# Kernel tuning notes

Measured on AMD Instinct MI355X. Metric: run time of the kernel, lower is better.

The kernel has to match this reference:

```python
import jax, jax.numpy as jnp
import numpy as np

DATA_SHAPE = (4, 32, 32)
K_EMBED_DIM = 64


def _local_stats(zf):
    # zf: [B, N]; torch std/var use ddof=1; torch.median returns lower median (sorted index (N-1)//2)
    n = zf.shape[1]
    mean = jnp.mean(zf, axis=1)
    var = jnp.var(zf, axis=1, ddof=1)
    std = jnp.sqrt(var)
    mn = jnp.min(zf, axis=1)
    mx = jnp.max(zf, axis=1)
    med = jnp.sort(zf, axis=1)[:, (n - 1) // 2]
    l2 = jnp.sqrt(jnp.sum(zf * zf, axis=1))
    l1 = jnp.sum(jnp.abs(zf), axis=1)
    pos = jnp.sum(zf > 0, axis=1).astype(zf.dtype)
    neg = jnp.sum(zf < 0, axis=1).astype(zf.dtype)
    return jnp.stack([mean, std, mn, mx, med, var, l2, l1, pos, neg], axis=1)


def _sinusoidal_embedding(k, dim):
    half = dim // 2
    freqs = jnp.exp(jnp.arange(half, dtype=jnp.float32) * (-np.log(10000.0) / (half - 1)))
    e = k * freqs
    return jnp.concatenate([jnp.sin(e), jnp.cos(e)], axis=0)  # [dim]


def _pos_encoding(t, f, s, max_scales):
    t = jnp.float32(t); f = jnp.float32(f)
    return jnp.stack([jnp.sin(0.1 * t), jnp.cos(0.1 * t), jnp.sin(0.1 * f), jnp.cos(0.1 * f),
                      jnp.float32(s) / jnp.float32(max_scales)])


def setup_inputs() -> dict:
    key = jax.random.key(0)
    ks = jax.random.split(key, 8)
    B = 8192
    input_dim = int(np.prod(DATA_SHAPE)) + K_EMBED_DIM + 5 + 10  # 4175
    def xavier(k, fan_in, fan_out):
        bound = np.sqrt(6.0 / (fan_in + fan_out))
        return jax.random.uniform(k, (fan_in, fan_out), jnp.float32, -bound, bound)
    return {
        "z_local": jax.random.normal(ks[0], (B,) + DATA_SHAPE, jnp.float32),
        "k": 500, "t": 10, "f": 20, "s": 2, "max_scales": 4,
        "W1": xavier(ks[1], input_dim, 256), "b1": jnp.zeros((256,), jnp.float32),
        "W2": xavier(ks[2], 256, 128), "b2": jnp.zeros((128,), jnp.float32),
        "W3": xavier(ks[3], 128, 64), "b3": jnp.zeros((64,), jnp.float32),
        "W4": xavier(ks[4], 64, 5), "b4": jnp.zeros((5,), jnp.float32),
    }


def reference(z_local, k, t, f, s, max_scales, W1, b1, W2, b2, W3, b3, W4, b4):
    B = z_local.shape[0]
    zf = z_local.reshape(B, -1)  # [B, 4096] == prod(data_shape), no pad/trim needed
    k_embed = _sinusoidal_embedding(k, K_EMBED_DIM)           # [64]
    pos_enc = _pos_encoding(t, f, s, max_scales)              # [5]
    stats = _local_stats(zf)                                  # [B, 10]
    feats = jnp.concatenate([
        zf,
        jnp.broadcast_to(k_embed[None, :], (B, K_EMBED_DIM)),
        jnp.broadcast_to(pos_enc[None, :], (B, 5)),
        stats,
    ], axis=1)
    h = jax.nn.relu(feats @ W1 + b1)
    h = jax.nn.relu(h @ W2 + b2)
    h = jax.nn.relu(h @ W3 + b3)
    logits = h @ W4 + b4
    return jax.nn.softmax(logits, axis=-1)
```

## Files before the change

kernel.cpp:

```cpp
#include <hip/hip_runtime.h>
#include <math.h>
#include <stdint.h>

#define DFEAT 4096
#define AS1 __attribute__((address_space(1)))
#define AS3 __attribute__((address_space(3)))

typedef _Float16 f16x8 __attribute__((ext_vector_type(8)));
typedef float f32x4 __attribute__((ext_vector_type(4)));

__global__ __launch_bounds__(256, 4) void stats_kernel(const float* __restrict__ z,
                                                       float* __restrict__ stats)
{
    const int lane = threadIdx.x & 63;
    const int wv   = threadIdx.x >> 6;
    const int row  = blockIdx.x * 4 + wv;
    const float* zr = z + (size_t)row * DFEAT;

    unsigned keys[64];
    float sum = 0.f, ss = 0.f, l1 = 0.f;
    float mn = INFINITY, mx = -INFINITY;
    int pos = 0, neg = 0;

    #pragma unroll
    for (int j = 0; j < 16; ++j) {
        float4 v = reinterpret_cast<const float4*>(zr)[lane + j * 64];
        float vv[4] = {v.x, v.y, v.z, v.w};
        #pragma unroll
        for (int e = 0; e < 4; ++e) {
            float x = vv[e];
            sum += x; ss += x * x; l1 += fabsf(x);
            mn = fminf(mn, x); mx = fmaxf(mx, x);
            pos += (x > 0.f) ? 1 : 0;
            neg += (x < 0.f) ? 1 : 0;
            unsigned u = __float_as_uint(x);
            keys[j * 4 + e] = (u & 0x80000000u) ? ~u : (u | 0x80000000u);
        }
    }

    #pragma unroll
    for (int off = 1; off < 64; off <<= 1) {
        sum += __shfl_xor(sum, off);
        ss  += __shfl_xor(ss,  off);
        l1  += __shfl_xor(l1,  off);
        mn = fminf(mn, __shfl_xor(mn, off));
        mx = fmaxf(mx, __shfl_xor(mx, off));
        pos += __shfl_xor(pos, off);
        neg += __shfl_xor(neg, off);
    }

    unsigned lo = 0u;
    const int t = (DFEAT - 1) / 2;
    #pragma unroll 1
    for (int b = 31; b >= 0; --b) {
        const unsigned mid = lo | (1u << b);
        int cnt = 0;
        #pragma unroll
        for (int i = 0; i < 64; ++i) cnt += (keys[i] < mid) ? 1 : 0;
        #pragma unroll
        for (int off = 1; off < 64; off <<= 1) cnt += __shfl_xor(cnt, off);
        if (cnt <= t) lo = mid;
    }

    if (lane == 0) {
        const float med = (lo & 0x80000000u) ? __uint_as_float(lo ^ 0x80000000u)
                                             : __uint_as_float(~lo);
        const float n = (float)DFEAT;
        const float mean = sum / n;
        const float var = (ss - sum * sum / n) / (n - 1.f);
        float* sp = stats + (size_t)row * 10;
        sp[0] = mean;
        sp[1] = sqrtf(var);
        sp[2] = mn;
        sp[3] = mx;
        sp[4] = med;
        sp[5] = var;
        sp[6] = sqrtf(ss);
        sp[7] = l1;
        sp[8] = (float)pos;
        sp[9] = (float)neg;
    }
}

__global__ __launch_bounds__(256) void split_kernel(const float* __restrict__ W1,
                                                    char* __restrict__ img)
{
    const int c   = blockIdx.x;
    const int col = threadIdx.x;
    const int k0  = c * 32;
    _Float16 h16[32], l16[32];
    #pragma unroll
    for (int kk = 0; kk < 32; ++kk) {
        float w = W1[(size_t)(k0 + kk) * 256 + col];
        _Float16 h = (_Float16)w;
        float rr = (w - (float)h) * 2048.f;
        h16[kk] = h;
        l16[kk] = (_Float16)rr;
    }
    char* base = img + (size_t)c * 32768;
    const int sw = (col >> 1) & 3;
    #pragma unroll
    for (int g = 0; g < 4; ++g) {
        f16x8 vh, vl;
        #pragma unroll
        for (int j = 0; j < 8; ++j) { vh[j] = h16[g * 8 + j]; vl[j] = l16[g * 8 + j]; }
        const int off = col * 64 + ((g ^ sw) << 4);
        *reinterpret_cast<f16x8*>(base + off)         = vh;
        *reinterpret_cast<f16x8*>(base + 16384 + off) = vl;
    }
}

__global__ __launch_bounds__(256) void prep_kernel(const int* kp, const int* tp,
                                                   const int* fp, const int* sp,
                                                   const int* msp,
                                                   const float* __restrict__ W1,
                                                   const float* __restrict__ b1,
                                                   float* __restrict__ cbias)
{
    __shared__ float ke[64];
    __shared__ float pe[5];
    const int tid = threadIdx.x;
    if (tid < 32) {
        const float c = (float)(-log(10000.0) / 31.0);
        const float freq = expf((float)tid * c);
        const float e = (float)(*kp) * freq;
        const double ed = (double)e;
        ke[tid]      = (float)sin(ed);
        ke[tid + 32] = (float)cos(ed);
    }
    if (tid == 0) {
        const float tf = (float)(*tp), ff = (float)(*fp);
        pe[0] = (float)sin((double)(0.1f * tf));
        pe[1] = (float)cos((double)(0.1f * tf));
        pe[2] = (float)sin((double)(0.1f * ff));
        pe[3] = (float)cos((double)(0.1f * ff));
        pe[4] = (float)(*sp) / (float)(*msp);
    }
    __syncthreads();
    float acc = b1[tid];
    #pragma unroll 8
    for (int i = 0; i < 64; ++i) acc += ke[i] * W1[(size_t)(4096 + i) * 256 + tid];
    #pragma unroll
    for (int i = 0; i < 5; ++i)  acc += pe[i] * W1[(size_t)(4160 + i) * 256 + tid];
    cbias[tid] = acc;
}

__global__ __launch_bounds__(256, 1) void mlp_kernel(
    const float* __restrict__ z, const char* __restrict__ img,
    const float* __restrict__ W1, const float* __restrict__ W2,
    const float* __restrict__ b2, const float* __restrict__ W3,
    const float* __restrict__ b3, const float* __restrict__ W4,
    const float* __restrict__ b4, const float* __restrict__ stats,
    const float* __restrict__ cbias, float* __restrict__ out)
{
    __shared__ char lds[65536];

    const int tid  = threadIdx.x;
    const int wv   = tid >> 6;
    const int r    = wv >> 1;
    const int cg   = wv & 1;
    const int lane = tid & 63;
    const int q    = lane & 15;
    const int g    = lane >> 4;
    const int row0 = blockIdx.x * 32;

    f32x4 acc0[8], acc1[8];
    #pragma unroll
    for (int f = 0; f < 8; ++f) {
        acc0[f] = (f32x4){0.f, 0.f, 0.f, 0.f};
        acc1[f] = (f32x4){0.f, 0.f, 0.f, 0.f};
    }

    const float* arow = z + (size_t)(row0 + 16 * r + q) * DFEAT + g * 8;
    const int sw = (q >> 1) & 3;

#define STAGE_B(T, DST) do {                                                   \
        const char* gsrc_ = img + (size_t)(T) * 32768 + wv * 8192 + lane * 16; \
        char* ldst_ = (DST) + wv * 8192;                                       \
        _Pragma("unroll")                                                      \
        for (int i_ = 0; i_ < 8; ++i_) {                                       \
            __builtin_amdgcn_global_load_lds(                                  \
                (const AS1 void*)(gsrc_ + i_ * 1024),                          \
                (AS3 void*)(ldst_ + i_ * 1024), 16, 0, 0);                     \
        }                                                                      \
    } while (0)

    float af[8];
    {
        STAGE_B(0, lds);
        float4 v0 = *reinterpret_cast<const float4*>(arow);
        float4 v1 = *reinterpret_cast<const float4*>(arow + 4);
        af[0] = v0.x; af[1] = v0.y; af[2] = v0.z; af[3] = v0.w;
        af[4] = v1.x; af[5] = v1.y; af[6] = v1.z; af[7] = v1.w;
    }
    __syncthreads();

    for (int tt = 0; tt < 128; ++tt) {
        char* buf  = lds + ((tt & 1) << 15);
        char* nbuf = lds + (((tt + 1) & 1) << 15);

        if (tt + 1 < 128) STAGE_B(tt + 1, nbuf);

        f16x8 ah, al;
        #pragma unroll
        for (int j = 0; j < 8; ++j) {
            _Float16 h = (_Float16)af[j];
            ah[j] = h;
            al[j] = (_Float16)((af[j] - (float)h) * 2048.f);
        }

        if (tt + 1 < 128) {
            const float* an = arow + (tt + 1) * 32;
            float4 v0 = *reinterpret_cast<const float4*>(an);
            float4 v1 = *reinterpret_cast<const float4*>(an + 4);
            af[0] = v0.x; af[1] = v0.y; af[2] = v0.z; af[3] = v0.w;
            af[4] = v1.x; af[5] = v1.y; af[6] = v1.z; af[7] = v1.w;
        }

        #pragma unroll
        for (int f = 0; f < 8; ++f) {
            const int colf = 128 * cg + 16 * f + q;
            const int off  = colf * 64 + ((g ^ sw) << 4);
            f16x8 bh = *reinterpret_cast<const f16x8*>(buf + off);
            f16x8 bl = *reinterpret_cast<const f16x8*>(buf + 16384 + off);
            acc0[f] = __builtin_amdgcn_mfma_f32_16x16x32_f16(ah, bh, acc0[f], 0, 0, 0);
            acc1[f] = __builtin_amdgcn_mfma_f32_16x16x32_f16(ah, bl, acc1[f], 0, 0, 0);
            acc1[f] = __builtin_amdgcn_mfma_f32_16x16x32_f16(al, bh, acc1[f], 0, 0, 0);
        }
        __syncthreads();
    }

    float* W1s_s   = reinterpret_cast<float*>(lds + 40000);
    float* stats_s = reinterpret_cast<float*>(lds + 50240);
    float* cb_s    = reinterpret_cast<float*>(lds + 51520);
    float* Hs      = reinterpret_cast<float*>(lds);

    for (int i = tid; i < 2560; i += 256) {
        const int s = i >> 8, cc = i & 255;
        W1s_s[i] = W1[(size_t)(4165 + s) * 256 + cc];
    }
    for (int i = tid; i < 320; i += 256)
        stats_s[i] = stats[(size_t)row0 * 10 + i];
    cb_s[tid] = cbias[tid];
    __syncthreads();

    #pragma unroll
    for (int j = 0; j < 4; ++j) {
        const int m = g * 4 + j;
        const int grow = 16 * r + m;
        float s10[10];
        #pragma unroll
        for (int s = 0; s < 10; ++s) s10[s] = stats_s[grow * 10 + s];
        #pragma unroll
        for (int f = 0; f < 8; ++f) {
            const int colf = 128 * cg + 16 * f + q;
            float h = acc0[f][j] + acc1[f][j] * (1.f / 2048.f) + cb_s[colf];
            #pragma unroll
            for (int s = 0; s < 10; ++s) h += s10[s] * W1s_s[s * 256 + colf];
            Hs[grow * 257 + colf] = fmaxf(h, 0.f);
        }
    }
    __syncthreads();

    float* H2 = reinterpret_cast<float*>(lds + 40000);
    {
        const int rr = tid >> 3;
        const int c0 = (tid & 7) * 16;
        float a2[16];
        #pragma unroll
        for (int i = 0; i < 16; ++i) a2[i] = b2[c0 + i];
        for (int k = 0; k < 256; ++k) {
            const float hv = Hs[rr * 257 + k];
            const float4 w0 = *reinterpret_cast<const float4*>(W2 + (size_t)k * 128 + c0);
            const float4 w1 = *reinterpret_cast<const float4*>(W2 + (size_t)k * 128 + c0 + 4);
            const float4 w2 = *reinterpret_cast<const float4*>(W2 + (size_t)k * 128 + c0 + 8);
            const float4 w3 = *reinterpret_cast<const float4*>(W2 + (size_t)k * 128 + c0 + 12);
            const float wvv[16] = {w0.x,w0.y,w0.z,w0.w, w1.x,w1.y,w1.z,w1.w,
                                   w2.x,w2.y,w2.z,w2.w, w3.x,w3.y,w3.z,w3.w};
            #pragma unroll
            for (int i = 0; i < 16; ++i) a2[i] += hv * wvv[i];
        }
        __syncthreads();
        #pragma unroll
        for (int i = 0; i < 16; ++i)
            H2[rr * 129 + c0 + i] = fmaxf(a2[i], 0.f);
    }
    __syncthreads();

    float* H3 = reinterpret_cast<float*>(lds + 56512);
    {
        const int rr = tid >> 3;
        const int c0 = (tid & 7) * 8;
        float a3[8];
        #pragma unroll
        for (int i = 0; i < 8; ++i) a3[i] = b3[c0 + i];
        for (int k = 0; k < 128; ++k) {
            const float hv = H2[rr * 129 + k];
            const float4 w0 = *reinterpret_cast<const float4*>(W3 + (size_t)k * 64 + c0);
            const float4 w1 = *reinterpret_cast<const float4*>(W3 + (size_t)k * 64 + c0 + 4);
            const float wvv[8] = {w0.x,w0.y,w0.z,w0.w, w1.x,w1.y,w1.z,w1.w};
            #pragma unroll
            for (int i = 0; i < 8; ++i) a3[i] += hv * wvv[i];
        }
        #pragma unroll
        for (int i = 0; i < 8; ++i)
            H3[rr * 65 + c0 + i] = fmaxf(a3[i], 0.f);
    }
    __syncthreads();

    if (tid < 32) {
        const int rr = tid;
        float lg[5];
        #pragma unroll
        for (int j = 0; j < 5; ++j) lg[j] = b4[j];
        for (int k = 0; k < 64; ++k) {
            const float hv = H3[rr * 65 + k];
            #pragma unroll
            for (int j = 0; j < 5; ++j) lg[j] += hv * W4[k * 5 + j];
        }
        float m = lg[0];
        #pragma unroll
        for (int j = 1; j < 5; ++j) m = fmaxf(m, lg[j]);
        float e[5], s = 0.f;
        #pragma unroll
        for (int j = 0; j < 5; ++j) { e[j] = expf(lg[j] - m); s += e[j]; }
        float* op = out + (size_t)(row0 + rr) * 5;
        #pragma unroll
        for (int j = 0; j < 5; ++j) op[j] = e[j] / s;
    }
#undef STAGE_B
}

extern "C" void kernel_launch(void* const* d_in, const int* in_sizes, int n_in,
                              void* d_out, int out_size, void* d_ws, size_t ws_size,
                              hipStream_t stream)
{
    const float* z   = (const float*)d_in[0];
    const int*   kp  = (const int*)d_in[1];
    const int*   tp  = (const int*)d_in[2];
    const int*   fp  = (const int*)d_in[3];
    const int*   sp  = (const int*)d_in[4];
    const int*   msp = (const int*)d_in[5];
    const float* W1  = (const float*)d_in[6];
    const float* b1  = (const float*)d_in[7];
    const float* W2  = (const float*)d_in[8];
    const float* b2  = (const float*)d_in[9];
    const float* W3  = (const float*)d_in[10];
    const float* b3  = (const float*)d_in[11];
    const float* W4  = (const float*)d_in[12];
    const float* b4  = (const float*)d_in[13];
    float* out = (float*)d_out;

    const int B = in_sizes[0] / DFEAT;
    float* ws_stats = (float*)d_ws;
    float* ws_cbias = ws_stats + (size_t)B * 10;
    char*  ws_img   = (char*)(ws_cbias + 256);

    hipLaunchKernelGGL(stats_kernel, dim3(B / 4), dim3(256), 0, stream, z, ws_stats);
    hipLaunchKernelGGL(split_kernel, dim3(128), dim3(256), 0, stream, W1, ws_img);
    hipLaunchKernelGGL(prep_kernel, dim3(1), dim3(256), 0, stream,
                       kp, tp, fp, sp, msp, W1, b1, ws_cbias);
    hipLaunchKernelGGL(mlp_kernel, dim3(B / 32), dim3(256), 0, stream,
                       z, ws_img, W1, W2, b2, W3, b3, W4, b4,
                       ws_stats, ws_cbias, out);
}
```

Before: 519.4 us.

## Deepen MLP B-operand pipeline to four LDS stages and split stats per block

The main GEMM loop moves from a double-buffered LDS ring with a full __syncthreads per chunk to a four-slot ring that keeps three chunks of W1 in flight, using explicit vmcnt waits and raw barriers, with A-row loads prefetched two chunks ahead. The aim is to hide global-to-LDS latency better in the memory-bound first layer, at the cost of 128 KB of LDS per block. Separately, the stats kernel now gives each row a whole 256-thread block instead of one wavefront. This cuts per-thread register keys from 64 to 16 but adds two block barriers per radix-select bit.

After: 504.5 us. 1.03x faster.

```diff
diff --git a/kernel.cpp b/kernel.cpp
--- a/kernel.cpp
+++ b/kernel.cpp
@@ -9,22 +9,26 @@
 typedef _Float16 f16x8 __attribute__((ext_vector_type(8)));
 typedef float f32x4 __attribute__((ext_vector_type(4)));
 
-__global__ __launch_bounds__(256, 4) void stats_kernel(const float* __restrict__ z,
-                                                       float* __restrict__ stats)
-{
-    const int lane = threadIdx.x & 63;
-    const int wv   = threadIdx.x >> 6;
-    const int row  = blockIdx.x * 4 + wv;
+__global__ __launch_bounds__(256) void stats_kernel(const float* __restrict__ z,
+                                                    float* __restrict__ stats)
+{
+    const int row  = blockIdx.x;
+    const int tid  = threadIdx.x;
+    const int lane = tid & 63;
+    const int wv   = tid >> 6;
+    __shared__ float wred[4][7];
+    __shared__ int   wcnt[4];
+
     const float* zr = z + (size_t)row * DFEAT;
 
-    unsigned keys[64];
+    unsigned keys[16];
     float sum = 0.f, ss = 0.f, l1 = 0.f;
     float mn = INFINITY, mx = -INFINITY;
     int pos = 0, neg = 0;
 
     #pragma unroll
-    for (int j = 0; j < 16; ++j) {
-        float4 v = reinterpret_cast<const float4*>(zr)[lane + j * 64];
+    for (int j = 0; j < 4; ++j) {
+        float4 v = reinterpret_cast<const float4*>(zr)[tid + j * 256];
         float vv[4] = {v.x, v.y, v.z, v.w};
         #pragma unroll
         for (int e = 0; e < 4; ++e) {
@@ -48,37 +52,54 @@
         pos += __shfl_xor(pos, off);
         neg += __shfl_xor(neg, off);
     }
+    if (lane == 0) {
+        wred[wv][0] = sum; wred[wv][1] = ss; wred[wv][2] = l1;
+        wred[wv][3] = mn;  wred[wv][4] = mx;
+        wred[wv][5] = (float)pos; wred[wv][6] = (float)neg;
+    }
+    __syncthreads();
 
     unsigned lo = 0u;
-    const int t = (DFEAT - 1) / 2;
     #pragma unroll 1
     for (int b = 31; b >= 0; --b) {
         const unsigned mid = lo | (1u << b);
-        int cnt = 0;
-        #pragma unroll
-        for (int i = 0; i < 64; ++i) cnt += (keys[i] < mid) ? 1 : 0;
-        #pragma unroll
-        for (int off = 1; off < 64; off <<= 1) cnt += __shfl_xor(cnt, off);
-        if (cnt <= t) lo = mid;
-    }
-
-    if (lane == 0) {
+        int c = 0;
+        #pragma unroll
+        for (int i = 0; i < 16; ++i) c += (keys[i] < mid) ? 1 : 0;
+        #pragma unroll
+        for (int off = 1; off < 64; off <<= 1) c += __shfl_xor(c, off);
+        if (lane == 0) wcnt[wv] = c;
+        __syncthreads();
+        const int tot = wcnt[0] + wcnt[1] + wcnt[2] + wcnt[3];
+        if (tot <= 2047) lo = mid;
+        __syncthreads();
+    }
+
+    if (tid == 0) {
+        float fsum = 0.f, fss = 0.f, fl1 = 0.f, fpos = 0.f, fneg = 0.f;
+        float fmn = INFINITY, fmx = -INFINITY;
+        #pragma unroll
+        for (int w = 0; w < 4; ++w) {
+            fsum += wred[w][0]; fss += wred[w][1]; fl1 += wred[w][2];
+            fmn = fminf(fmn, wred[w][3]); fmx = fmaxf(fmx, wred[w][4]);
+            fpos += wred[w][5]; fneg += wred[w][6];
+        }
         const float med = (lo & 0x80000000u) ? __uint_as_float(lo ^ 0x80000000u)
                                              : __uint_as_float(~lo);
         const float n = (float)DFEAT;
-        const float mean = sum / n;
-        const float var = (ss - sum * sum / n) / (n - 1.f);
+        const float mean = fsum / n;
+        const float var = (fss - fsum * fsum / n) / (n - 1.f);
         float* sp = stats + (size_t)row * 10;
         sp[0] = mean;
         sp[1] = sqrtf(var);
-        sp[2] = mn;
-        sp[3] = mx;
+        sp[2] = fmn;
+        sp[3] = fmx;
         sp[4] = med;
         sp[5] = var;
-        sp[6] = sqrtf(ss);
-        sp[7] = l1;
-        sp[8] = (float)pos;
-        sp[9] = (float)neg;
+        sp[6] = sqrtf(fss);
+        sp[7] = fl1;
+        sp[8] = fpos;
+        sp[9] = fneg;
     }
 }
 
@@ -153,7 +174,7 @@
     const float* __restrict__ b4, const float* __restrict__ stats,
     const float* __restrict__ cbias, float* __restrict__ out)
 {
-    __shared__ char lds[65536];
+    __shared__ char lds[131072];
 
     const int tid  = threadIdx.x;
     const int wv   = tid >> 6;
@@ -174,61 +195,65 @@
     const float* arow = z + (size_t)(row0 + 16 * r + q) * DFEAT + g * 8;
     const int sw = (q >> 1) & 3;
 
-#define STAGE_B(T, DST) do {                                                   \
-        const char* gsrc_ = img + (size_t)(T) * 32768 + wv * 8192 + lane * 16; \
-        char* ldst_ = (DST) + wv * 8192;                                       \
+    auto STAGE = [&](int chunk, int slot) {
+        const char* gsrc = img + (size_t)chunk * 32768 + wv * 8192 + lane * 16;
+        char* ldst = lds + (slot << 15) + wv * 8192;
+        #pragma unroll
+        for (int i = 0; i < 8; ++i)
+            __builtin_amdgcn_global_load_lds((const AS1 void*)(gsrc + i * 1024),
+                                             (AS3 void*)(ldst + i * 1024), 16, 0, 0);
+    };
+    auto LOADA = [&](int chunk, float4& v0, float4& v1) {
+        const float* an = arow + chunk * 32;
+        v0 = *reinterpret_cast<const float4*>(an);
+        v1 = *reinterpret_cast<const float4*>(an + 4);
+    };
+
+    float4 aA0, aA1, aB0, aB1;
+    STAGE(0, 0);
+    STAGE(1, 1);
+    LOADA(0, aA0, aA1);
+    STAGE(2, 2);
+    LOADA(1, aB0, aB1);
+
+#define CHUNK_BODY(T, Av0, Av1) do {                                           \
+        asm volatile("s_waitcnt vmcnt(10)" ::: "memory");                      \
+        __builtin_amdgcn_s_barrier();                                          \
+        STAGE(((T) + 3) & 127, ((T) + 3) & 3);                                 \
+        f16x8 ah, al;                                                          \
+        {                                                                      \
+            const float afv[8] = {Av0.x, Av0.y, Av0.z, Av0.w,                  \
+                                  Av1.x, Av1.y, Av1.z, Av1.w};                 \
+            _Pragma("unroll")                                                  \
+            for (int j = 0; j < 8; ++j) {                                      \
+                _Float16 h = (_Float16)afv[j];                                 \
+                ah[j] = h;                                                     \
+                al[j] = (_Float16)((afv[j] - (float)h) * 2048.f);              \
+            }                                                                  \
+        }                                                                      \
+        LOADA(((T) + 2) & 127, Av0, Av1);                                      \
+        const char* buf = lds + (((T) & 3) << 15);                             \
         _Pragma("unroll")                                                      \
-        for (int i_ = 0; i_ < 8; ++i_) {                                       \
-            __builtin_amdgcn_global_load_lds(                                  \
-                (const AS1 void*)(gsrc_ + i_ * 1024),                          \
-                (AS3 void*)(ldst_ + i_ * 1024), 16, 0, 0);                     \
+        for (int f = 0; f < 8; ++f) {                                          \
+            const int colf = 128 * cg + 16 * f + q;                            \
+            const int off  = colf * 64 + ((g ^ sw) << 4);                      \
+            f16x8 bh = *reinterpret_cast<const f16x8*>(buf + off);             \
+            f16x8 bl = *reinterpret_cast<const f16x8*>(buf + 16384 + off);     \
+            acc0[f] = __builtin_amdgcn_mfma_f32_16x16x32_f16(ah, bh, acc0[f], 0, 0, 0); \
+            acc1[f] = __builtin_amdgcn_mfma_f32_16x16x32_f16(ah, bl, acc1[f], 0, 0, 0); \
+            acc1[f] = __builtin_amdgcn_mfma_f32_16x16x32_f16(al, bh, acc1[f], 0, 0, 0); \
         }                                                                      \
     } while (0)
 
-    float af[8];
-    {
-        STAGE_B(0, lds);
-        float4 v0 = *reinterpret_cast<const float4*>(arow);
-        float4 v1 = *reinterpret_cast<const float4*>(arow + 4);
-        af[0] = v0.x; af[1] = v0.y; af[2] = v0.z; af[3] = v0.w;
-        af[4] = v1.x; af[5] = v1.y; af[6] = v1.z; af[7] = v1.w;
-    }
-    __syncthreads();
-
-    for (int tt = 0; tt < 128; ++tt) {
-        char* buf  = lds + ((tt & 1) << 15);
-        char* nbuf = lds + (((tt + 1) & 1) << 15);
-
-        if (tt + 1 < 128) STAGE_B(tt + 1, nbuf);
-
-        f16x8 ah, al;
-        #pragma unroll
-        for (int j = 0; j < 8; ++j) {
-            _Float16 h = (_Float16)af[j];
-            ah[j] = h;
-            al[j] = (_Float16)((af[j] - (float)h) * 2048.f);
-        }
-
-        if (tt + 1 < 128) {
-            const float* an = arow + (tt + 1) * 32;
-            float4 v0 = *reinterpret_cast<const float4*>(an);
-            float4 v1 = *reinterpret_cast<const float4*>(an + 4);
-            af[0] = v0.x; af[1] = v0.y; af[2] = v0.z; af[3] = v0.w;
-            af[4] = v1.x; af[5] = v1.y; af[6] = v1.z; af[7] = v1.w;
-        }
-
-        #pragma unroll
-        for (int f = 0; f < 8; ++f) {
-            const int colf = 128 * cg + 16 * f + q;
-            const int off  = colf * 64 + ((g ^ sw) << 4);
-            f16x8 bh = *reinterpret_cast<const f16x8*>(buf + off);
-            f16x8 bl = *reinterpret_cast<const f16x8*>(buf + 16384 + off);
-            acc0[f] = __builtin_amdgcn_mfma_f32_16x16x32_f16(ah, bh, acc0[f], 0, 0, 0);
-            acc1[f] = __builtin_amdgcn_mfma_f32_16x16x32_f16(ah, bl, acc1[f], 0, 0, 0);
-            acc1[f] = __builtin_amdgcn_mfma_f32_16x16x32_f16(al, bh, acc1[f], 0, 0, 0);
-        }
-        __syncthreads();
-    }
+    #pragma unroll 1
+    for (int u = 0; u < 64; ++u) {
+        const int t0 = 2 * u;
+        CHUNK_BODY(t0, aA0, aA1);
+        CHUNK_BODY(t0 + 1, aB0, aB1);
+    }
+#undef CHUNK_BODY
+
+    __syncthreads();
 
     float* W1s_s   = reinterpret_cast<float*>(lds + 40000);
     float* stats_s = reinterpret_cast<float*>(lds + 50240);
@@ -328,7 +353,6 @@
         #pragma unroll
         for (int j = 0; j < 5; ++j) op[j] = e[j] / s;
     }
-#undef STAGE_B
 }
 
 extern "C" void kernel_launch(void* const* d_in, const int* in_sizes, int n_in,
@@ -356,7 +380,7 @@
     float* ws_cbias = ws_stats + (size_t)B * 10;
     char*  ws_img   = (char*)(ws_cbias + 256);
 
-    hipLaunchKernelGGL(stats_kernel, dim3(B / 4), dim3(256), 0, stream, z, ws_stats);
+    hipLaunchKernelGGL(stats_kernel, dim3(B), dim3(256), 0, stream, z, ws_stats);
     hipLaunchKernelGGL(split_kernel, dim3(128), dim3(256), 0, stream, W1, ws_img);
     hipLaunchKernelGGL(prep_kernel, dim3(1), dim3(256), 0, stream,
                        kp, tp, fp, sp, msp, W1, b1, ws_cbias);
```

## Split K across two wave groups in MLP kernel and use ballot-popcount median

Applied to the files above, without the earlier changes.

The main GEMM kernel now uses 512 threads, with two halves each covering half of the 4096-long K dimension. Each wave computes two row tiles over 64 columns, and the partial sums are reduced through LDS before the epilogue. The LDS double buffer grows to 128KB, which halves the number of K iterations per wave and doubles the waves available to hide latency, but limits how many blocks fit per CU. The stats kernel replaces the per-bit shuffle-reduction count in the radix median search with ballot+popcount and relaxes its launch bounds and unroll, which cuts cross-lane reduction cost.

Result: faster. 463.7 us (-10.7%).

```diff
diff --git a/kernel.cpp b/kernel.cpp
--- a/kernel.cpp
+++ b/kernel.cpp
@@ -9,8 +9,8 @@
 typedef _Float16 f16x8 __attribute__((ext_vector_type(8)));
 typedef float f32x4 __attribute__((ext_vector_type(4)));
 
-__global__ __launch_bounds__(256, 4) void stats_kernel(const float* __restrict__ z,
-                                                       float* __restrict__ stats)
+__global__ __launch_bounds__(256) void stats_kernel(const float* __restrict__ z,
+                                                    float* __restrict__ stats)
 {
     const int lane = threadIdx.x & 63;
     const int wv   = threadIdx.x >> 6;
@@ -22,7 +22,7 @@
     float mn = INFINITY, mx = -INFINITY;
     int pos = 0, neg = 0;
 
-    #pragma unroll
+    #pragma unroll 4
     for (int j = 0; j < 16; ++j) {
         float4 v = reinterpret_cast<const float4*>(zr)[lane + j * 64];
         float vv[4] = {v.x, v.y, v.z, v.w};
@@ -50,16 +50,14 @@
     }
 
     unsigned lo = 0u;
-    const int t = (DFEAT - 1) / 2;
     #pragma unroll 1
     for (int b = 31; b >= 0; --b) {
         const unsigned mid = lo | (1u << b);
         int cnt = 0;
         #pragma unroll
-        for (int i = 0; i < 64; ++i) cnt += (keys[i] < mid) ? 1 : 0;
-        #pragma unroll
-        for (int off = 1; off < 64; off <<= 1) cnt += __shfl_xor(cnt, off);
-        if (cnt <= t) lo = mid;
+        for (int i = 0; i < 64; ++i)
+            cnt += (int)__popcll(__ballot(keys[i] < mid));
+        if (cnt <= 2047) lo = mid;
     }
 
     if (lane == 0) {
@@ -145,7 +143,7 @@
     cbias[tid] = acc;
 }
 
-__global__ __launch_bounds__(256, 1) void mlp_kernel(
+__global__ __launch_bounds__(512, 2) void mlp_kernel(
     const float* __restrict__ z, const char* __restrict__ img,
     const float* __restrict__ W1, const float* __restrict__ W2,
     const float* __restrict__ b2, const float* __restrict__ W3,
@@ -153,157 +151,180 @@
     const float* __restrict__ b4, const float* __restrict__ stats,
     const float* __restrict__ cbias, float* __restrict__ out)
 {
-    __shared__ char lds[65536];
+    __shared__ char lds[131072];
 
     const int tid  = threadIdx.x;
     const int wv   = tid >> 6;
-    const int r    = wv >> 1;
-    const int cg   = wv & 1;
+    const int kh   = wv >> 2;
+    const int wc   = wv & 3;
     const int lane = tid & 63;
     const int q    = lane & 15;
     const int g    = lane >> 4;
     const int row0 = blockIdx.x * 32;
 
-    f32x4 acc0[8], acc1[8];
-    #pragma unroll
-    for (int f = 0; f < 8; ++f) {
-        acc0[f] = (f32x4){0.f, 0.f, 0.f, 0.f};
-        acc1[f] = (f32x4){0.f, 0.f, 0.f, 0.f};
-    }
-
-    const float* arow = z + (size_t)(row0 + 16 * r + q) * DFEAT + g * 8;
+    f32x4 acc0[2][4], acc1[2][4];
+    #pragma unroll
+    for (int rt = 0; rt < 2; ++rt)
+        #pragma unroll
+        for (int f = 0; f < 4; ++f) {
+            acc0[rt][f] = (f32x4){0.f, 0.f, 0.f, 0.f};
+            acc1[rt][f] = (f32x4){0.f, 0.f, 0.f, 0.f};
+        }
+
+    const float* arow0 = z + (size_t)(row0 + q) * DFEAT + kh * 2048 + g * 8;
+    const float* arow1 = arow0 + (size_t)16 * DFEAT;
     const int sw = (q >> 1) & 3;
 
-#define STAGE_B(T, DST) do {                                                   \
-        const char* gsrc_ = img + (size_t)(T) * 32768 + wv * 8192 + lane * 16; \
-        char* ldst_ = (DST) + wv * 8192;                                       \
-        _Pragma("unroll")                                                      \
-        for (int i_ = 0; i_ < 8; ++i_) {                                       \
-            __builtin_amdgcn_global_load_lds(                                  \
-                (const AS1 void*)(gsrc_ + i_ * 1024),                          \
-                (AS3 void*)(ldst_ + i_ * 1024), 16, 0, 0);                     \
-        }                                                                      \
-    } while (0)
-
-    float af[8];
-    {
-        STAGE_B(0, lds);
-        float4 v0 = *reinterpret_cast<const float4*>(arow);
-        float4 v1 = *reinterpret_cast<const float4*>(arow + 4);
-        af[0] = v0.x; af[1] = v0.y; af[2] = v0.z; af[3] = v0.w;
-        af[4] = v1.x; af[5] = v1.y; af[6] = v1.z; af[7] = v1.w;
-    }
-    __syncthreads();
-
-    for (int tt = 0; tt < 128; ++tt) {
-        char* buf  = lds + ((tt & 1) << 15);
-        char* nbuf = lds + (((tt + 1) & 1) << 15);
-
-        if (tt + 1 < 128) STAGE_B(tt + 1, nbuf);
-
-        f16x8 ah, al;
-        #pragma unroll
-        for (int j = 0; j < 8; ++j) {
-            _Float16 h = (_Float16)af[j];
-            ah[j] = h;
-            al[j] = (_Float16)((af[j] - (float)h) * 2048.f);
-        }
-
-        if (tt + 1 < 128) {
-            const float* an = arow + (tt + 1) * 32;
-            float4 v0 = *reinterpret_cast<const float4*>(an);
-            float4 v1 = *reinterpret_cast<const float4*>(an + 4);
-            af[0] = v0.x; af[1] = v0.y; af[2] = v0.z; af[3] = v0.w;
-            af[4] = v1.x; af[5] = v1.y; af[6] = v1.z; af[7] = v1.w;
-        }
-
-        #pragma unroll
-        for (int f = 0; f < 8; ++f) {
-            const int colf = 128 * cg + 16 * f + q;
+    auto STAGE = [&](int t, char* dst) {
+        const char* s0 = img + ((size_t)t << 15) + tid * 16;
+        const char* s1 = img + ((size_t)(t + 64) << 15) + tid * 16;
+        #pragma unroll
+        for (int i = 0; i < 4; ++i) {
+            __builtin_amdgcn_global_load_lds((const AS1 void*)(s0 + i * 8192),
+                                             (AS3 void*)(dst + i * 8192 + tid * 16), 16, 0, 0);
+            __builtin_amdgcn_global_load_lds((const AS1 void*)(s1 + i * 8192),
+                                             (AS3 void*)(dst + 32768 + i * 8192 + tid * 16), 16, 0, 0);
+        }
+    };
+
+    float4 a00, a01, a10, a11;
+    auto LOADA = [&](int t) {
+        const float* p0 = arow0 + t * 32;
+        const float* p1 = arow1 + t * 32;
+        a00 = *reinterpret_cast<const float4*>(p0);
+        a01 = *reinterpret_cast<const float4*>(p0 + 4);
+        a10 = *reinterpret_cast<const float4*>(p1);
+        a11 = *reinterpret_cast<const float4*>(p1 + 4);
+    };
+
+    STAGE(0, lds);
+    LOADA(0);
+    __syncthreads();
+
+    for (int t = 0; t < 64; ++t) {
+        char* buf  = lds + ((t & 1) << 16);
+        char* nbuf = lds + (((t + 1) & 1) << 16);
+        if (t + 1 < 64) STAGE(t + 1, nbuf);
+
+        f16x8 ah0, al0, ah1, al1;
+        {
+            const float f0[8] = {a00.x, a00.y, a00.z, a00.w, a01.x, a01.y, a01.z, a01.w};
+            const float f1[8] = {a10.x, a10.y, a10.z, a10.w, a11.x, a11.y, a11.z, a11.w};
+            #pragma unroll
+            for (int j = 0; j < 8; ++j) {
+                _Float16 h0 = (_Float16)f0[j];
+                ah0[j] = h0;
+                al0[j] = (_Float16)((f0[j] - (float)h0) * 2048.f);
+                _Float16 h1 = (_Float16)f1[j];
+                ah1[j] = h1;
+                al1[j] = (_Float16)((f1[j] - (float)h1) * 2048.f);
+            }
+        }
+        if (t + 1 < 64) LOADA(t + 1);
+
+        const char* bb = buf + kh * 32768;
+        #pragma unroll
+        for (int f = 0; f < 4; ++f) {
+            const int colf = 64 * wc + 16 * f + q;
             const int off  = colf * 64 + ((g ^ sw) << 4);
-            f16x8 bh = *reinterpret_cast<const f16x8*>(buf + off);
-            f16x8 bl = *reinterpret_cast<const f16x8*>(buf + 16384 + off);
-            acc0[f] = __builtin_amdgcn_mfma_f32_16x16x32_f16(ah, bh, acc0[f], 0, 0, 0);
-            acc1[f] = __builtin_amdgcn_mfma_f32_16x16x32_f16(ah, bl, acc1[f], 0, 0, 0);
-            acc1[f] = __builtin_amdgcn_mfma_f32_16x16x32_f16(al, bh, acc1[f], 0, 0, 0);
+            f16x8 bh = *reinterpret_cast<const f16x8*>(bb + off);
+            f16x8 bl = *reinterpret_cast<const f16x8*>(bb + 16384 + off);
+            acc0[0][f] = __builtin_amdgcn_mfma_f32_16x16x32_f16(ah0, bh, acc0[0][f], 0, 0, 0);
+            acc1[0][f] = __builtin_amdgcn_mfma_f32_16x16x32_f16(ah0, bl, acc1[0][f], 0, 0, 0);
+            acc1[0][f] = __builtin_amdgcn_mfma_f32_16x16x32_f16(al0, bh, acc1[0][f], 0, 0, 0);
+            acc0[1][f] = __builtin_amdgcn_mfma_f32_16x16x32_f16(ah1, bh, acc0[1][f], 0, 0, 0);
+            acc1[1][f] = __builtin_amdgcn_mfma_f32_16x16x32_f16(ah1, bl, acc1[1][f], 0, 0, 0);
+            acc1[1][f] = __builtin_amdgcn_mfma_f32_16x16x32_f16(al1, bh, acc1[1][f], 0, 0, 0);
         }
         __syncthreads();
     }
 
-    float* W1s_s   = reinterpret_cast<float*>(lds + 40000);
-    float* stats_s = reinterpret_cast<float*>(lds + 50240);
-    float* cb_s    = reinterpret_cast<float*>(lds + 51520);
-    float* Hs      = reinterpret_cast<float*>(lds);
-
-    for (int i = tid; i < 2560; i += 256) {
+    float* P_s     = reinterpret_cast<float*>(lds);
+    float* Hs      = reinterpret_cast<float*>(lds + 32768);
+    float* W1s_s   = reinterpret_cast<float*>(lds + 65664);
+    float* stats_s = reinterpret_cast<float*>(lds + 75904);
+    float* cb_s    = reinterpret_cast<float*>(lds + 77184);
+    float* H2      = reinterpret_cast<float*>(lds + 78208);
+    float* H3      = reinterpret_cast<float*>(lds + 94720);
+
+    if (kh == 1) {
+        #pragma unroll
+        for (int rt = 0; rt < 2; ++rt)
+            #pragma unroll
+            for (int j = 0; j < 4; ++j) {
+                const int grow = 16 * rt + 4 * g + j;
+                #pragma unroll
+                for (int f = 0; f < 4; ++f) {
+                    const int colf = 64 * wc + 16 * f + q;
+                    P_s[grow * 256 + colf] = acc0[rt][f][j] + acc1[rt][f][j] * (1.f / 2048.f);
+                }
+            }
+    }
+    for (int i = tid; i < 2560; i += 512) {
         const int s = i >> 8, cc = i & 255;
         W1s_s[i] = W1[(size_t)(4165 + s) * 256 + cc];
     }
-    for (int i = tid; i < 320; i += 256)
-        stats_s[i] = stats[(size_t)row0 * 10 + i];
-    cb_s[tid] = cbias[tid];
-    __syncthreads();
-
-    #pragma unroll
-    for (int j = 0; j < 4; ++j) {
-        const int m = g * 4 + j;
-        const int grow = 16 * r + m;
-        float s10[10];
-        #pragma unroll
-        for (int s = 0; s < 10; ++s) s10[s] = stats_s[grow * 10 + s];
-        #pragma unroll
-        for (int f = 0; f < 8; ++f) {
-            const int colf = 128 * cg + 16 * f + q;
-            float h = acc0[f][j] + acc1[f][j] * (1.f / 2048.f) + cb_s[colf];
-            #pragma unroll
-            for (int s = 0; s < 10; ++s) h += s10[s] * W1s_s[s * 256 + colf];
-            Hs[grow * 257 + colf] = fmaxf(h, 0.f);
-        }
-    }
-    __syncthreads();
-
-    float* H2 = reinterpret_cast<float*>(lds + 40000);
+    if (tid < 320) stats_s[tid] = stats[(size_t)row0 * 10 + tid];
+    if (tid < 256) cb_s[tid] = cbias[tid];
+    __syncthreads();
+
+    if (kh == 0) {
+        #pragma unroll
+        for (int rt = 0; rt < 2; ++rt)
+            #pragma unroll
+            for (int j = 0; j < 4; ++j) {
+                const int grow = 16 * rt + 4 * g + j;
+                float s10[10];
+                #pragma unroll
+                for (int s = 0; s < 10; ++s) s10[s] = stats_s[grow * 10 + s];
+                #pragma unroll
+                for (int f = 0; f < 4; ++f) {
+                    const int colf = 64 * wc + 16 * f + q;
+                    float h = acc0[rt][f][j] + acc1[rt][f][j] * (1.f / 2048.f)
+                            + P_s[grow * 256 + colf] + cb_s[colf];
+                    #pragma unroll
+                    for (int s = 0; s < 10; ++s) h += s10[s] * W1s_s[s * 256 + colf];
+                    Hs[grow * 257 + colf] = fmaxf(h, 0.f);
+                }
+            }
+    }
+    __syncthreads();
+
     {
-        const int rr = tid >> 3;
-        const int c0 = (tid & 7) * 16;
-        float a2[16];
-        #pragma unroll
-        for (int i = 0; i < 16; ++i) a2[i] = b2[c0 + i];
+        const int rr = tid >> 4;
+        const int c0 = (tid & 15) * 8;
+        float a2[8];
+        #pragma unroll
+        for (int i = 0; i < 8; ++i) a2[i] = b2[c0 + i];
         for (int k = 0; k < 256; ++k) {
             const float hv = Hs[rr * 257 + k];
             const float4 w0 = *reinterpret_cast<const float4*>(W2 + (size_t)k * 128 + c0);
             const float4 w1 = *reinterpret_cast<const float4*>(W2 + (size_t)k * 128 + c0 + 4);
-            const float4 w2 = *reinterpret_cast<const float4*>(W2 + (size_t)k * 128 + c0 + 8);
-            const float4 w3 = *reinterpret_cast<const float4*>(W2 + (size_t)k * 128 + c0 + 12);
-            const float wvv[16] = {w0.x,w0.y,w0.z,w0.w, w1.x,w1.y,w1.z,w1.w,
-                                   w2.x,w2.y,w2.z,w2.w, w3.x,w3.y,w3.z,w3.w};
-            #pragma unroll
-            for (int i = 0; i < 16; ++i) a2[i] += hv * wvv[i];
-        }
-        __syncthreads();
-        #pragma unroll
-        for (int i = 0; i < 16; ++i)
+            const float wvv[8] = {w0.x,w0.y,w0.z,w0.w, w1.x,w1.y,w1.z,w1.w};
+            #pragma unroll
+            for (int i = 0; i < 8; ++i) a2[i] += hv * wvv[i];
+        }
+        #pragma unroll
+        for (int i = 0; i < 8; ++i)
             H2[rr * 129 + c0 + i] = fmaxf(a2[i], 0.f);
     }
     __syncthreads();
 
-    float* H3 = reinterpret_cast<float*>(lds + 56512);
     {
-        const int rr = tid >> 3;
-        const int c0 = (tid & 7) * 8;
-        float a3[8];
-        #pragma unroll
-        for (int i = 0; i < 8; ++i) a3[i] = b3[c0 + i];
+        const int rr = tid >> 4;
+        const int c0 = (tid & 15) * 4;
+        float a3[4];
+        #pragma unroll
+        for (int i = 0; i < 4; ++i) a3[i] = b3[c0 + i];
         for (int k = 0; k < 128; ++k) {
             const float hv = H2[rr * 129 + k];
             const float4 w0 = *reinterpret_cast<const float4*>(W3 + (size_t)k * 64 + c0);
-            const float4 w1 = *reinterpret_cast<const float4*>(W3 + (size_t)k * 64 + c0 + 4);
-            const float wvv[8] = {w0.x,w0.y,w0.z,w0.w, w1.x,w1.y,w1.z,w1.w};
-            #pragma unroll
-            for (int i = 0; i < 8; ++i) a3[i] += hv * wvv[i];
-        }
-        #pragma unroll
-        for (int i = 0; i < 8; ++i)
+            const float wvv[4] = {w0.x, w0.y, w0.z, w0.w};
+            #pragma unroll
+            for (int i = 0; i < 4; ++i) a3[i] += hv * wvv[i];
+        }
+        #pragma unroll
+        for (int i = 0; i < 4; ++i)
             H3[rr * 65 + c0 + i] = fmaxf(a3[i], 0.f);
     }
     __syncthreads();
@@ -328,7 +349,6 @@
         #pragma unroll
         for (int j = 0; j < 5; ++j) op[j] = e[j] / s;
     }
-#undef STAGE_B
 }
 
 extern "C" void kernel_launch(void* const* d_in, const int* in_sizes, int n_in,
@@ -360,7 +380,7 @@
     hipLaunchKernelGGL(split_kernel, dim3(128), dim3(256), 0, stream, W1, ws_img);
     hipLaunchKernelGGL(prep_kernel, dim3(1), dim3(256), 0, stream,
                        kp, tp, fp, sp, msp, W1, b1, ws_cbias);
-    hipLaunchKernelGGL(mlp_kernel, dim3(B / 32), dim3(256), 0, stream,
+    hipLaunchKernelGGL(mlp_kernel, dim3(B / 32), dim3(512), 0, stream,
                        z, ws_img, W1, W2, b2, W3, b3, W4, b4,
                        ws_stats, ws_cbias, out);
 }
```
